# Kernel optimization log

Measured on AMD Instinct MI355X. Metric: run time of the kernel, lower is better.

## Reference

```python
import jax, jax.numpy as jnp
import numpy as np

B, C, H, W = 8, 256, 64, 64


def setup_inputs() -> dict:
    key = jax.random.key(0)
    kx, kq, kk, kv, kp = jax.random.split(key, 5)
    scale = 1.0 / np.sqrt(C)  # ~conv2d default init scale
    return {
        "X": jax.random.normal(kx, (B, C, H, W), jnp.float32),
        "Wq": jax.random.normal(kq, (C, C), jnp.float32) * scale,
        "Wk": jax.random.normal(kk, (C, C), jnp.float32) * scale,
        "Wv": jax.random.normal(kv, (C, C), jnp.float32) * scale,
        "Wp": jax.random.normal(kp, (C, C), jnp.float32) * scale,
    }


def _conv1x1(Wt, X):
    # 1x1 conv without bias == channel-mixing matmul. W: (out_c, in_c)
    return jnp.einsum('oc,bchw->bohw', Wt, X)


def reference(X, Wq, Wk, Wv, Wp):
    b, c, h, w = X.shape
    hw = h * w
    # NOTE: the original torch code uses .view (reinterpret) NOT transpose,
    # so q/v are reshaped from (B,C,HW) row-major directly into (B,HW,C).
    q = _conv1x1(Wq, X).reshape(b, hw, c)
    k = _conv1x1(Wk, X).reshape(b, c, hw)
    v = _conv1x1(Wv, X).reshape(b, hw, c)
    wei = jax.nn.softmax(jnp.matmul(q, k) / jnp.sqrt(jnp.asarray(c, X.dtype)), axis=-1)  # (B,HW,HW)
    out = jnp.matmul(wei, v).reshape(b, c, h, w)
    return _conv1x1(Wp, out)
```

## Files before the change

### kernel.cpp

```cpp
#include <hip/hip_runtime.h>
#include <hip/hip_fp16.h>


using half8  = _Float16 __attribute__((ext_vector_type(8)));
using half4v = _Float16 __attribute__((ext_vector_type(4)));
using f32x4  = float    __attribute__((ext_vector_type(4)));

#define HWC 1048576

#define G2L(gp, lp)                                                   \
  __builtin_amdgcn_global_load_lds(                                   \
      (const __attribute__((address_space(1))) void*)(gp),            \
      (__attribute__((address_space(3))) void*)(lp), 16, 0, 0)

__global__ void k_convert_w(const float* __restrict__ wq, const float* __restrict__ wk,
                            const float* __restrict__ wv, const float* __restrict__ wp,
                            _Float16* __restrict__ out) {
  int idx = (blockIdx.x * 256 + threadIdx.x) * 4;
  const float* src = idx < 65536 ? wq : idx < 131072 ? wk : idx < 196608 ? wv : wp;
  float4 v = *reinterpret_cast<const float4*>(src + (idx & 65535));
  half4v h = { (_Float16)v.x, (_Float16)v.y, (_Float16)v.z, (_Float16)v.w };
  *reinterpret_cast<half4v*>(out + idx) = h;
}

__global__ void k_transpose_f32(const float* __restrict__ in, _Float16* __restrict__ out,
                                int R, int S) {
  size_t base = (size_t)blockIdx.z * R * S;
  in += base; out += base;
  int r0 = blockIdx.y * 64, s0 = blockIdx.x * 64;
  __shared__ _Float16 tile[4096];
  char* tb = (char*)tile;
  int t = threadIdx.x;
#pragma unroll
  for (int i = 0; i < 4; ++i) {
    int row = i * 16 + (t >> 4);
    int co  = t & 15;
    float4 v = *reinterpret_cast<const float4*>(in + (size_t)(r0 + row) * S + s0 + co * 4);
    float vv[4] = {v.x, v.y, v.z, v.w};
#pragma unroll
    for (int e = 0; e < 4; ++e) {
      int sl = co * 4 + e;
      int byte = (sl * 128 + row * 2) ^ (((sl >> 3) & 7) << 4);
      *reinterpret_cast<_Float16*>(tb + byte) = (_Float16)vv[e];
    }
  }
  __syncthreads();
#pragma unroll
  for (int i = 0; i < 2; ++i) {
    int so  = i * 32 + (t >> 3);
    int co2 = t & 7;
    int byte = (so * 128 + co2 * 16) ^ (((so >> 3) & 7) << 4);
    uint4 v = *reinterpret_cast<const uint4*>(tb + byte);
    *reinterpret_cast<uint4*>(out + (size_t)(s0 + so) * R + r0 + co2 * 8) = v;
  }
}

__global__ void k_transpose_h16(const _Float16* __restrict__ in, _Float16* __restrict__ out,
                                int R, int S) {
  size_t base = (size_t)blockIdx.z * R * S;
  in += base; out += base;
  int r0 = blockIdx.y * 64, s0 = blockIdx.x * 64;
  __shared__ _Float16 tile[4096];
  char* tb = (char*)tile;
  int t = threadIdx.x;
#pragma unroll
  for (int i = 0; i < 2; ++i) {
    int row = i * 32 + (t >> 3);
    int co  = t & 7;
    half8 v = *reinterpret_cast<const half8*>(in + (size_t)(r0 + row) * S + s0 + co * 8);
#pragma unroll
    for (int e = 0; e < 8; ++e) {
      int sl = co * 8 + e;
      int byte = (sl * 128 + row * 2) ^ (((sl >> 3) & 7) << 4);
      *reinterpret_cast<_Float16*>(tb + byte) = v[e];
    }
  }
  __syncthreads();
#pragma unroll
  for (int i = 0; i < 2; ++i) {
    int so  = i * 32 + (t >> 3);
    int co2 = t & 7;
    int byte = (so * 128 + co2 * 16) ^ (((so >> 3) & 7) << 4);
    uint4 v = *reinterpret_cast<const uint4*>(tb + byte);
    *reinterpret_cast<uint4*>(out + (size_t)(s0 + so) * R + r0 + co2 * 8) = v;
  }
}

template <bool OUT_F32>
__global__ __launch_bounds__(256) void k_gemm(const _Float16* __restrict__ A,
                                              const _Float16* __restrict__ Bt,
                                              void* __restrict__ Yv, int M, int N,
                                              long sA, long sB, long sY, float scale) {
  int b = blockIdx.z;
  A  += (size_t)b * sA;
  Bt += (size_t)b * sB;
  int n0 = blockIdx.x * 64, m0 = blockIdx.y * 64;
  int t = threadIdx.x, wave = t >> 6, lane = t & 63;
  int lm = lane & 15, lk8 = (lane >> 4) * 8;
  int nr = n0 + wave * 16 + lm;
  f32x4 zero = {0.f, 0.f, 0.f, 0.f};
  f32x4 acc[4] = {zero, zero, zero, zero};
#pragma unroll
  for (int ks = 0; ks < 8; ++ks) {
    half8 bf = *reinterpret_cast<const half8*>(Bt + (size_t)nr * 256 + ks * 32 + lk8);
#pragma unroll
    for (int mt = 0; mt < 4; ++mt) {
      half8 af = *reinterpret_cast<const half8*>(A + (size_t)(m0 + mt * 16 + lm) * 256 + ks * 32 + lk8);
      acc[mt] = __builtin_amdgcn_mfma_f32_16x16x32_f16(af, bf, acc[mt], 0, 0, 0);
    }
  }
  int rq = (lane >> 4) * 4;
#pragma unroll
  for (int mt = 0; mt < 4; ++mt) {
#pragma unroll
    for (int r = 0; r < 4; ++r) {
      size_t off = (size_t)(m0 + mt * 16 + rq + r) * N + n0 + wave * 16 + lm;
      float v = acc[mt][r] * scale;
      if (OUT_F32) reinterpret_cast<float*>(Yv)[(size_t)b * sY + off] = v;
      else reinterpret_cast<_Float16*>(Yv)[(size_t)b * sY + off] = (_Float16)v;
    }
  }
}

__global__ __launch_bounds__(256, 2) void k_attn(const _Float16* __restrict__ Q,
                                                 const _Float16* __restrict__ Kt,
                                                 const _Float16* __restrict__ Vt,
                                                 _Float16* __restrict__ O) {
  extern __shared__ char lds[];
  int wg = blockIdx.x;
  int b = wg & 7, qt = wg >> 3;
  const _Float16* Qb  = Q  + (size_t)b * HWC;
  const _Float16* Ktb = Kt + (size_t)b * HWC;
  const _Float16* Vtb = Vt + (size_t)b * HWC;
  _Float16* Ob = O + (size_t)b * HWC;
  int t = threadIdx.x, wave = t >> 6, lane = t & 63;
  int lm = lane & 15, lkb = lane >> 4;
  int q0 = qt * 64 + wave * 16;
  char* Plds = lds + wave * 2048;

  half8 qf[8];
#pragma unroll
  for (int ks = 0; ks < 8; ++ks)
    qf[ks] = *reinterpret_cast<const half8*>(Qb + (size_t)(q0 + lm) * 256 + ks * 32 + lkb * 8);

  f32x4 zero = {0.f, 0.f, 0.f, 0.f};
  f32x4 oacc[16];
#pragma unroll
  for (int i = 0; i < 16; ++i) oacc[i] = zero;
  float mrun[4] = {-1e30f, -1e30f, -1e30f, -1e30f};
  float lrun[4] = {0.f, 0.f, 0.f, 0.f};

#pragma unroll 1
  for (int kb = 0; kb < 64; ++kb) {
#pragma unroll
    for (int i = 0; i < 8; ++i) {
      int c = i * 256 + t;
      int sk = (c ^ ((c >> 5) & 7)) * 8;
      G2L(Ktb + (size_t)kb * 16384 + sk, lds + i * 4096 + wave * 1024);
    }
#pragma unroll
    for (int i = 0; i < 8; ++i) {
      int c = i * 256 + t;
      int ch = c >> 3, cov = (c & 7) ^ (ch & 7);
      G2L(Vtb + (size_t)ch * 4096 + kb * 64 + cov * 8, lds + 32768 + i * 4096 + wave * 1024);
    }
    __syncthreads();

    f32x4 sacc[4] = {zero, zero, zero, zero};
#pragma unroll
    for (int nt = 0; nt < 4; ++nt) {
      int krow = nt * 16 + lm;
#pragma unroll
      for (int ks = 0; ks < 8; ++ks) {
        half8 kf = *reinterpret_cast<const half8*>(
            lds + ((krow * 512 + ks * 64 + lkb * 16) ^ ((krow & 7) << 4)));
        sacc[nt] = __builtin_amdgcn_mfma_f32_16x16x32_f16(qf[ks], kf, sacc[nt], 0, 0, 0);
      }
    }
    __syncthreads();

    float p[4][4], mnew[4], alpha[4];
#pragma unroll
    for (int r = 0; r < 4; ++r) {
      float mx = fmaxf(fmaxf(sacc[0][r], sacc[1][r]), fmaxf(sacc[2][r], sacc[3][r]));
#pragma unroll
      for (int m = 1; m < 16; m <<= 1) mx = fmaxf(mx, __shfl_xor(mx, m, 64));
      mnew[r] = fmaxf(mrun[r], mx);
      alpha[r] = exp2f((mrun[r] - mnew[r]) * 1.4426950408889634f);
      mrun[r] = mnew[r];
    }
#pragma unroll
    for (int r = 0; r < 4; ++r) {
      float s = 0.f;
#pragma unroll
      for (int nt = 0; nt < 4; ++nt) {
        p[nt][r] = exp2f((sacc[nt][r] - mnew[r]) * 1.4426950408889634f);
        s += p[nt][r];
      }
#pragma unroll
      for (int m = 1; m < 16; m <<= 1) s += __shfl_xor(s, m, 64);
      lrun[r] = lrun[r] * alpha[r] + s;
    }
#pragma unroll
    for (int ct = 0; ct < 16; ++ct)
#pragma unroll
      for (int r = 0; r < 4; ++r) oacc[ct][r] *= alpha[r];

#pragma unroll
    for (int nt = 0; nt < 4; ++nt) {
#pragma unroll
      for (int r = 0; r < 4; ++r) {
        int prow = lkb * 4 + r, key = nt * 16 + lm;
        *reinterpret_cast<_Float16*>(Plds + ((prow * 128 + key * 2) ^ ((prow & 7) << 4))) =
            (_Float16)p[nt][r];
      }
    }

#pragma unroll
    for (int ks2 = 0; ks2 < 2; ++ks2) {
      half8 pf = *reinterpret_cast<const half8*>(
          Plds + ((lm * 128 + ks2 * 64 + lkb * 16) ^ ((lm & 7) << 4)));
#pragma unroll
      for (int ct = 0; ct < 16; ++ct) {
        int vrow = ct * 16 + lm;
        half8 vf = *reinterpret_cast<const half8*>(
            lds + 32768 + ((vrow * 128 + ks2 * 64 + lkb * 16) ^ ((vrow & 7) << 4)));
        oacc[ct] = __builtin_amdgcn_mfma_f32_16x16x32_f16(pf, vf, oacc[ct], 0, 0, 0);
      }
    }
    __syncthreads();
  }

  float inv[4];
#pragma unroll
  for (int r = 0; r < 4; ++r) inv[r] = 1.0f / lrun[r];
#pragma unroll
  for (int ct = 0; ct < 16; ++ct) {
#pragma unroll
    for (int r = 0; r < 4; ++r) {
      Ob[(size_t)(q0 + lkb * 4 + r) * 256 + ct * 16 + lm] = (_Float16)(oacc[ct][r] * inv[r]);
    }
  }
}

extern "C" void kernel_launch(void* const* d_in, const int* in_sizes, int n_in,
                              void* d_out, int out_size, void* d_ws, size_t ws_size,
                              hipStream_t stream) {
  (void)in_sizes; (void)n_in; (void)out_size; (void)ws_size;
  const float* X  = (const float*)d_in[0];
  const float* Wq = (const float*)d_in[1];
  const float* Wk = (const float*)d_in[2];
  const float* Wv = (const float*)d_in[3];
  const float* Wp = (const float*)d_in[4];

  char* ws = (char*)d_ws;
  _Float16* Wbf = (_Float16*)ws;
  _Float16* Xt  = (_Float16*)(ws + (1ull  << 20));
  _Float16* Qb  = (_Float16*)(ws + (17ull << 20));
  _Float16* Ktb = (_Float16*)(ws + (33ull << 20));
  _Float16* Vc  = (_Float16*)(ws + (49ull << 20));
  _Float16* Vtb = Xt;
  _Float16* Ob  = Vc;
  _Float16* Lb  = Qb;

  k_convert_w<<<256, 256, 0, stream>>>(Wq, Wk, Wv, Wp, Wbf);
  k_transpose_f32<<<dim3(64, 4, 8), 256, 0, stream>>>(X, Xt, 256, 4096);
  k_gemm<false><<<dim3(64, 4, 8), 256, 0, stream>>>(Wbf, Xt, Qb, 256, 4096, 0, HWC, HWC, 0.0625f);
  k_gemm<false><<<dim3(4, 64, 8), 256, 0, stream>>>(Xt, Wbf + 65536, Ktb, 4096, 256, HWC, 0, HWC, 1.0f);
  k_gemm<false><<<dim3(64, 4, 8), 256, 0, stream>>>(Wbf + 131072, Xt, Vc, 256, 4096, 0, HWC, HWC, 1.0f);
  k_transpose_h16<<<dim3(4, 64, 8), 256, 0, stream>>>(Vc, Vtb, 4096, 256);
  k_attn<<<512, 256, 65536, stream>>>(Qb, Ktb, Vtb, Ob);
  k_transpose_h16<<<dim3(64, 4, 8), 256, 0, stream>>>(Ob, Lb, 256, 4096);
  k_gemm<true><<<dim3(64, 4, 8), 256, 0, stream>>>(Wbf + 196608, Lb, d_out, 256, 4096, 0, HWC, HWC, 1.0f);
}
```

Before: 547.2 us.

## Rewrite attention with 32x32 MFMA, double-buffered KV, register P, lazy rescale

```diff
diff --git a/kernel.cpp b/kernel.cpp
--- a/kernel.cpp
+++ b/kernel.cpp
@@ -5,6 +5,7 @@
 using half8  = _Float16 __attribute__((ext_vector_type(8)));
 using half4v = _Float16 __attribute__((ext_vector_type(4)));
 using f32x4  = float    __attribute__((ext_vector_type(4)));
+using f32x16 = float    __attribute__((ext_vector_type(16)));
 
 #define HWC 1048576
 
@@ -134,112 +135,112 @@
   const _Float16* Vtb = Vt + (size_t)b * HWC;
   _Float16* Ob = O + (size_t)b * HWC;
   int t = threadIdx.x, wave = t >> 6, lane = t & 63;
-  int lm = lane & 15, lkb = lane >> 4;
-  int q0 = qt * 64 + wave * 16;
-  char* Plds = lds + wave * 2048;
-
-  half8 qf[8];
-#pragma unroll
-  for (int ks = 0; ks < 8; ++ks)
-    qf[ks] = *reinterpret_cast<const half8*>(Qb + (size_t)(q0 + lm) * 256 + ks * 32 + lkb * 8);
-
-  f32x4 zero = {0.f, 0.f, 0.f, 0.f};
-  f32x4 oacc[16];
-#pragma unroll
-  for (int i = 0; i < 16; ++i) oacc[i] = zero;
-  float mrun[4] = {-1e30f, -1e30f, -1e30f, -1e30f};
-  float lrun[4] = {0.f, 0.f, 0.f, 0.f};
+  int lq = lane & 31, hi = lane >> 5;
+  int q0 = qt * 128 + wave * 32;
+
+  half8 qf[16];
+#pragma unroll
+  for (int ks = 0; ks < 16; ++ks)
+    qf[ks] = *reinterpret_cast<const half8*>(Qb + (size_t)(q0 + lq) * 256 + ks * 16 + hi * 8);
+
+  f32x16 oacc[8] = {};
+  float mrun = -1e30f, lrun = 0.f;
+
+#define STAGEKV(kb_, base_)                                                        \
+  {                                                                                \
+    _Pragma("unroll") for (int i = 0; i < 4; ++i) {                                \
+      int c = i * 256 + t;                                                         \
+      int key = c >> 5, co = c & 31;                                               \
+      G2L(Ktb + (size_t)((kb_) * 32 + key) * 256 + ((co ^ (key & 7)) * 8),         \
+          lds + (base_) + (i * 256 + wave * 64) * 16);                             \
+    }                                                                              \
+    _Pragma("unroll") for (int i = 0; i < 4; ++i) {                                \
+      int c = i * 256 + t;                                                         \
+      int ch = c >> 2, ko = c & 3;                                                 \
+      G2L(Vtb + (size_t)ch * 4096 + (kb_) * 32 + ((ko ^ ((ch >> 1) & 3)) * 8),     \
+          lds + (base_) + 16384 + (i * 256 + wave * 64) * 16);                     \
+    }                                                                              \
+  }
+
+  STAGEKV(0, 0);
+  __syncthreads();
+  int cur = 0;
 
 #pragma unroll 1
-  for (int kb = 0; kb < 64; ++kb) {
-#pragma unroll
-    for (int i = 0; i < 8; ++i) {
-      int c = i * 256 + t;
-      int sk = (c ^ ((c >> 5) & 7)) * 8;
-      G2L(Ktb + (size_t)kb * 16384 + sk, lds + i * 4096 + wave * 1024);
-    }
-#pragma unroll
-    for (int i = 0; i < 8; ++i) {
-      int c = i * 256 + t;
-      int ch = c >> 3, cov = (c & 7) ^ (ch & 7);
-      G2L(Vtb + (size_t)ch * 4096 + kb * 64 + cov * 8, lds + 32768 + i * 4096 + wave * 1024);
-    }
+  for (int kb = 0; kb < 128; ++kb) {
+    if (kb < 127) STAGEKV(kb + 1, (cur ^ 1) * 32768);
+
+    const char* Kl = lds + cur * 32768;
+    const char* Vl = lds + cur * 32768 + 16384;
+
+    f32x16 sacc = {};
+#pragma unroll
+    for (int ks = 0; ks < 16; ++ks) {
+      half8 kf = *reinterpret_cast<const half8*>(
+          Kl + ((lq * 512 + ks * 32 + hi * 16) ^ ((lq & 7) << 4)));
+      sacc = __builtin_amdgcn_mfma_f32_32x32x16_f16(kf, qf[ks], sacc, 0, 0, 0);
+    }
+
+    float pmax = sacc[0];
+#pragma unroll
+    for (int r = 1; r < 16; ++r) pmax = fmaxf(pmax, sacc[r]);
+    pmax = fmaxf(pmax, __shfl_xor(pmax, 32));
+    if (__any(pmax > mrun + 8.0f)) {
+      float mnew = fmaxf(mrun, pmax);
+      float al = exp2f(mrun - mnew);
+      lrun *= al;
+#pragma unroll
+      for (int r = 0; r < 16; ++r) {
+        float ap = __shfl(al, ((r & 3) + 8 * (r >> 2) + 4 * hi) | (lane & 32));
+#pragma unroll
+        for (int nt = 0; nt < 8; ++nt) oacc[nt][r] *= ap;
+      }
+      mrun = mnew;
+    }
+    float p[16], s = 0.f;
+#pragma unroll
+    for (int r = 0; r < 16; ++r) { p[r] = exp2f(sacc[r] - mrun); s += p[r]; }
+    s += __shfl_xor(s, 32);
+    lrun += s;
+
+    unsigned own[8];
+#pragma unroll
+    for (int m = 0; m < 8; ++m)
+      own[m] = __builtin_bit_cast(unsigned,
+                 __builtin_amdgcn_cvt_pkrtz(p[2 * m], p[2 * m + 1]));
+    unsigned prt[8];
+#pragma unroll
+    for (int m = 0; m < 8; ++m) prt[m] = (unsigned)__shfl_xor((int)own[m], 32);
+    uint4 w0 = make_uint4(hi ? prt[2] : own[0], hi ? prt[3] : own[1],
+                          hi ? own[2] : prt[0], hi ? own[3] : prt[1]);
+    uint4 w1 = make_uint4(hi ? prt[6] : own[4], hi ? prt[7] : own[5],
+                          hi ? own[6] : prt[4], hi ? own[7] : prt[5]);
+    half8 pa0 = __builtin_bit_cast(half8, w0);
+    half8 pa1 = __builtin_bit_cast(half8, w1);
+
+#pragma unroll
+    for (int nt = 0; nt < 8; ++nt) {
+      int ch = nt * 32 + lq;
+      int sw = ((ch >> 1) & 3) << 4;
+      half8 v0 = *reinterpret_cast<const half8*>(Vl + ((ch * 64 + hi * 16) ^ sw));
+      oacc[nt] = __builtin_amdgcn_mfma_f32_32x32x16_f16(pa0, v0, oacc[nt], 0, 0, 0);
+      half8 v1 = *reinterpret_cast<const half8*>(Vl + ((ch * 64 + 32 + hi * 16) ^ sw));
+      oacc[nt] = __builtin_amdgcn_mfma_f32_32x32x16_f16(pa1, v1, oacc[nt], 0, 0, 0);
+    }
+
     __syncthreads();
-
-    f32x4 sacc[4] = {zero, zero, zero, zero};
-#pragma unroll
-    for (int nt = 0; nt < 4; ++nt) {
-      int krow = nt * 16 + lm;
-#pragma unroll
-      for (int ks = 0; ks < 8; ++ks) {
-        half8 kf = *reinterpret_cast<const half8*>(
-            lds + ((krow * 512 + ks * 64 + lkb * 16) ^ ((krow & 7) << 4)));
-        sacc[nt] = __builtin_amdgcn_mfma_f32_16x16x32_f16(qf[ks], kf, sacc[nt], 0, 0, 0);
-      }
-    }
-    __syncthreads();
-
-    float p[4][4], mnew[4], alpha[4];
-#pragma unroll
-    for (int r = 0; r < 4; ++r) {
-      float mx = fmaxf(fmaxf(sacc[0][r], sacc[1][r]), fmaxf(sacc[2][r], sacc[3][r]));
-#pragma unroll
-      for (int m = 1; m < 16; m <<= 1) mx = fmaxf(mx, __shfl_xor(mx, m, 64));
-      mnew[r] = fmaxf(mrun[r], mx);
-      alpha[r] = exp2f((mrun[r] - mnew[r]) * 1.4426950408889634f);
-      mrun[r] = mnew[r];
-    }
-#pragma unroll
-    for (int r = 0; r < 4; ++r) {
-      float s = 0.f;
-#pragma unroll
-      for (int nt = 0; nt < 4; ++nt) {
-        p[nt][r] = exp2f((sacc[nt][r] - mnew[r]) * 1.4426950408889634f);
-        s += p[nt][r];
-      }
-#pragma unroll
-      for (int m = 1; m < 16; m <<= 1) s += __shfl_xor(s, m, 64);
-      lrun[r] = lrun[r] * alpha[r] + s;
-    }
-#pragma unroll
-    for (int ct = 0; ct < 16; ++ct)
-#pragma unroll
-      for (int r = 0; r < 4; ++r) oacc[ct][r] *= alpha[r];
-
-#pragma unroll
-    for (int nt = 0; nt < 4; ++nt) {
-#pragma unroll
-      for (int r = 0; r < 4; ++r) {
-        int prow = lkb * 4 + r, key = nt * 16 + lm;
-        *reinterpret_cast<_Float16*>(Plds + ((prow * 128 + key * 2) ^ ((prow & 7) << 4))) =
-            (_Float16)p[nt][r];
-      }
-    }
-
-#pragma unroll
-    for (int ks2 = 0; ks2 < 2; ++ks2) {
-      half8 pf = *reinterpret_cast<const half8*>(
-          Plds + ((lm * 128 + ks2 * 64 + lkb * 16) ^ ((lm & 7) << 4)));
-#pragma unroll
-      for (int ct = 0; ct < 16; ++ct) {
-        int vrow = ct * 16 + lm;
-        half8 vf = *reinterpret_cast<const half8*>(
-            lds + 32768 + ((vrow * 128 + ks2 * 64 + lkb * 16) ^ ((vrow & 7) << 4)));
-        oacc[ct] = __builtin_amdgcn_mfma_f32_16x16x32_f16(pf, vf, oacc[ct], 0, 0, 0);
-      }
-    }
-    __syncthreads();
-  }
-
-  float inv[4];
-#pragma unroll
-  for (int r = 0; r < 4; ++r) inv[r] = 1.0f / lrun[r];
-#pragma unroll
-  for (int ct = 0; ct < 16; ++ct) {
-#pragma unroll
-    for (int r = 0; r < 4; ++r) {
-      Ob[(size_t)(q0 + lkb * 4 + r) * 256 + ct * 16 + lm] = (_Float16)(oacc[ct][r] * inv[r]);
-    }
+    cur ^= 1;
+  }
+#undef STAGEKV
+
+  float li = 1.0f / lrun;
+#pragma unroll
+  for (int r = 0; r < 16; ++r) {
+    int qrow = (r & 3) + 8 * (r >> 2) + 4 * hi;
+    float lv = __shfl(li, qrow | (lane & 32));
+    _Float16* dst = Ob + (size_t)(q0 + qrow) * 256 + lq;
+#pragma unroll
+    for (int nt = 0; nt < 8; ++nt) dst[nt * 32] = (_Float16)(oacc[nt][r] * lv);
   }
 }
 
@@ -265,11 +266,12 @@
 
   k_convert_w<<<256, 256, 0, stream>>>(Wq, Wk, Wv, Wp, Wbf);
   k_transpose_f32<<<dim3(64, 4, 8), 256, 0, stream>>>(X, Xt, 256, 4096);
-  k_gemm<false><<<dim3(64, 4, 8), 256, 0, stream>>>(Wbf, Xt, Qb, 256, 4096, 0, HWC, HWC, 0.0625f);
+  k_gemm<false><<<dim3(64, 4, 8), 256, 0, stream>>>(Wbf, Xt, Qb, 256, 4096, 0, HWC, HWC,
+                                                    0.0625f * 1.4426950408889634f);
   k_gemm<false><<<dim3(4, 64, 8), 256, 0, stream>>>(Xt, Wbf + 65536, Ktb, 4096, 256, HWC, 0, HWC, 1.0f);
   k_gemm<false><<<dim3(64, 4, 8), 256, 0, stream>>>(Wbf + 131072, Xt, Vc, 256, 4096, 0, HWC, HWC, 1.0f);
   k_transpose_h16<<<dim3(4, 64, 8), 256, 0, stream>>>(Vc, Vtb, 4096, 256);
-  k_attn<<<512, 256, 65536, stream>>>(Qb, Ktb, Vtb, Ob);
+  k_attn<<<256, 256, 65536, stream>>>(Qb, Ktb, Vtb, Ob);
   k_transpose_h16<<<dim3(64, 4, 8), 256, 0, stream>>>(Ob, Lb, 256, 4096);
   k_gemm<true><<<dim3(64, 4, 8), 256, 0, stream>>>(Wbf + 196608, Lb, d_out, 256, 4096, 0, HWC, HWC, 1.0f);
 }
```

New measurement: 606.2 us. 1.11x slower.
